# Kernel optimization log

Measured on AMD Instinct MI355X. Metric: run time of the kernel, lower is better.

Reference implementation:

```python
import jax, jax.numpy as jnp
import numpy as np

N = 50000
E = 800000
HID = 128
NH = 8
DH = HID // NH


def setup_inputs() -> dict:
    key = jax.random.key(0)
    ks = jax.random.split(key, 12)
    h = jax.random.normal(ks[0], (N, HID), dtype=jnp.float32)
    row = jnp.sort(jax.random.randint(ks[1], (E,), 0, N))
    col = jax.random.randint(ks[2], (E,), 0, N)
    s = 1.0 / np.sqrt(HID)
    Wq = jax.random.uniform(ks[3], (HID, HID), jnp.float32, -s, s)
    bq = jax.random.uniform(ks[4], (HID,), jnp.float32, -s, s)
    Wk = jax.random.uniform(ks[5], (HID, HID), jnp.float32, -s, s)
    bk = jax.random.uniform(ks[6], (HID,), jnp.float32, -s, s)
    Wv = jax.random.uniform(ks[7], (HID, HID), jnp.float32, -s, s)
    bv = jax.random.uniform(ks[8], (HID,), jnp.float32, -s, s)
    Wo = jax.random.uniform(ks[9], (HID, HID), jnp.float32, -s, s)
    bo = jax.random.uniform(ks[10], (HID,), jnp.float32, -s, s)
    return {"h": h, "row": row, "col": col, "Wq": Wq, "bq": bq,
            "Wk": Wk, "bk": bk, "Wv": Wv, "bv": bv, "Wo": Wo, "bo": bo}


def reference(h, row, col, Wq, bq, Wk, bk, Wv, bv, Wo, bo):
    n = h.shape[0]
    # projections; torch view(N, dh, nh): heads are the fastest-varying axis
    q = (h @ Wq.T + bq).reshape(n, DH, NH)
    k = (h @ Wk.T + bk).reshape(n, DH, NH)
    v = (h @ Wv.T + bv).reshape(n, DH, NH)
    # sddmm: per-edge score[e, head] = sum_d q[row_e, d, head] * k[col_e, d, head]
    scores = jnp.einsum('edh,edh->eh', q[row], k[col]) / np.sqrt(DH)
    # sparse softmax over each row's neighbors (dim=1)
    m = jax.ops.segment_max(scores, row, num_segments=n)       # [N, nh]
    e = jnp.exp(scores - m[row])                               # [E, nh]
    z = jax.ops.segment_sum(e, row, num_segments=n)            # [N, nh]
    attn = e / z[row]
    # bspmm: out[i] = sum_{j in N(i)} attn[ij] * v[j]
    out = jax.ops.segment_sum(attn[:, None, :] * v[col], row, num_segments=n)
    out = out.reshape(n, HID)
    return out @ Wo.T + bo
```

## Files before the change

### kernel.cpp

```cpp
#include <hip/hip_runtime.h>
#include <hip/hip_bf16.h>
#include <math.h>

#define HID 128
#define NH 8
#define DH 16

typedef __bf16 bf16x8 __attribute__((ext_vector_type(8)));
typedef float  f32x4  __attribute__((ext_vector_type(4)));

__global__ void prep_kernel(const int* __restrict__ row, int* __restrict__ row_ptr,
                            int N_, int E_,
                            const float* __restrict__ Wq, const float* __restrict__ Wk,
                            const float* __restrict__ Wv, const float* __restrict__ Wo,
                            const float* __restrict__ bq, const float* __restrict__ bk,
                            const float* __restrict__ bv,
                            __bf16* __restrict__ Whi, __bf16* __restrict__ Wlo,
                            float* __restrict__ bias384) {
    int idx = blockIdx.x * blockDim.x + threadIdx.x;
    if (idx < 4 * 16384) {
        int j = idx >> 14;
        int rem = idx & 16383;
        const float* W = (j == 0) ? Wq : (j == 1) ? Wk : (j == 2) ? Wv : Wo;
        float x = W[rem];
        __bf16 hv = (__bf16)x;
        Whi[idx] = hv;
        Wlo[idx] = (__bf16)(x - (float)hv);
    }
    if (idx <= N_) {
        int lo = 0, hi = E_;
        while (lo < hi) {
            int mid = (lo + hi) >> 1;
            if (row[mid] < idx) lo = mid + 1; else hi = mid;
        }
        row_ptr[idx] = lo;
    }
    if (idx < 384) {
        int j = idx >> 7;
        int pcol = idx & 127;
        int o = ((pcol & 15) << 3) | (pcol >> 4);
        const float* b = (j == 0) ? bq : (j == 1) ? bk : bv;
        bias384[idx] = b[o];
    }
}

__global__ __launch_bounds__(256)
void qkv_mfma_kernel(const float* __restrict__ h, int M,
                     const __bf16* __restrict__ Whi, const __bf16* __restrict__ Wlo,
                     const float* __restrict__ bias384,
                     float* __restrict__ q, __bf16* __restrict__ kv) {
    __shared__ __bf16 As2[2][64 * 128];
    int tid  = threadIdx.x;
    int wv   = tid >> 6;
    int lane = tid & 63;
    int r    = lane & 15;
    int kg   = lane >> 4;
    int m0   = blockIdx.x * 64;
    int colbase = wv * 96;

    #pragma unroll
    for (int it = 0; it < 4; ++it) {
        int flat = it * 256 + tid;
        int row  = flat >> 4;
        int s    = flat & 15;
        int g    = s ^ (row & 7);
        int grow = m0 + row; if (grow > M - 1) grow = M - 1;
        const float* src = &h[(size_t)grow * 128 + g * 8];
        float4 x0 = *(const float4*)src;
        float4 x1 = *(const float4*)(src + 4);
        float xs[8] = {x0.x, x0.y, x0.z, x0.w, x1.x, x1.y, x1.z, x1.w};
        bf16x8 hv8, lv8;
        #pragma unroll
        for (int e = 0; e < 8; ++e) {
            __bf16 hv = (__bf16)xs[e];
            hv8[e] = hv;
            lv8[e] = (__bf16)(xs[e] - (float)hv);
        }
        *(bf16x8*)&As2[0][row * 128 + s * 8] = hv8;
        *(bf16x8*)&As2[1][row * 128 + s * 8] = lv8;
    }
    __syncthreads();

    f32x4 acc[6][4];
    #pragma unroll
    for (int cf = 0; cf < 6; ++cf)
        #pragma unroll
        for (int rf = 0; rf < 4; ++rf)
            acc[cf][rf] = (f32x4){0.f, 0.f, 0.f, 0.f};

    int wrow[6];
    #pragma unroll
    for (int cf = 0; cf < 6; ++cf) {
        int col  = colbase + cf * 16 + r;
        int j    = col >> 7;
        int pcol = col & 127;
        int o    = ((pcol & 15) << 3) | (pcol >> 4);
        wrow[cf] = (j * 128 + o) * 128;
    }

    #pragma unroll
    for (int t = 0; t < 4; ++t) {
        int k0   = t * 32 + kg * 8;
        int slot = t * 4 + kg;
        bf16x8 bh[6], bl[6];
        #pragma unroll
        for (int cf = 0; cf < 6; ++cf) {
            bh[cf] = *(const bf16x8*)&Whi[wrow[cf] + k0];
            bl[cf] = *(const bf16x8*)&Wlo[wrow[cf] + k0];
        }
        bf16x8 ah[4], al[4];
        #pragma unroll
        for (int rf = 0; rf < 4; ++rf) {
            int row = rf * 16 + r;
            int s2  = slot ^ (r & 7);
            ah[rf] = *(bf16x8*)&As2[0][row * 128 + s2 * 8];
            al[rf] = *(bf16x8*)&As2[1][row * 128 + s2 * 8];
        }
        #pragma unroll
        for (int cf = 0; cf < 6; ++cf) {
            #pragma unroll
            for (int rf = 0; rf < 4; ++rf) {
                acc[cf][rf] = __builtin_amdgcn_mfma_f32_16x16x32_bf16(ah[rf], bh[cf], acc[cf][rf], 0, 0, 0);
                acc[cf][rf] = __builtin_amdgcn_mfma_f32_16x16x32_bf16(al[rf], bh[cf], acc[cf][rf], 0, 0, 0);
                acc[cf][rf] = __builtin_amdgcn_mfma_f32_16x16x32_bf16(ah[rf], bl[cf], acc[cf][rf], 0, 0, 0);
            }
        }
    }

    __syncthreads();
    __bf16* kvs = &As2[0][0];
    int orow = kg * 4;
    #pragma unroll
    for (int cf = 0; cf < 6; ++cf) {
        int col  = colbase + cf * 16 + r;
        int j    = col >> 7;
        int pcol = col & 127;
        float b  = bias384[col];
        #pragma unroll
        for (int rf = 0; rf < 4; ++rf) {
            #pragma unroll
            for (int e = 0; e < 4; ++e) {
                int mrow = rf * 16 + orow + e;
                float val = acc[cf][rf][e] + b;
                if (j == 0) {
                    int mg = m0 + mrow;
                    if (mg < M) q[(size_t)mg * 128 + pcol] = val;
                } else {
                    int gi  = pcol >> 2;
                    int idx = gi * 8 + ((j == 1) ? 0 : 4) + (pcol & 3);
                    kvs[mrow * 256 + idx] = (__bf16)val;
                }
            }
        }
    }
    __syncthreads();
    #pragma unroll
    for (int it = 0; it < 8; ++it) {
        int flat = it * 256 + tid;
        int row  = flat >> 5;
        int c    = flat & 31;
        int mg   = m0 + row;
        if (mg < M)
            *(uint4*)&kv[(size_t)mg * 256 + c * 8] = *(uint4*)&kvs[row * 256 + c * 8];
    }
}

__device__ __forceinline__ float blo(unsigned u) { return __uint_as_float(u << 16); }
__device__ __forceinline__ float bhi(unsigned u) { return __uint_as_float(u & 0xffff0000u); }

__global__ __launch_bounds__(256)
void edge_attn_kernel(const int* __restrict__ row_ptr, const int* __restrict__ col,
                      const float* __restrict__ q, const __bf16* __restrict__ kv,
                      float* __restrict__ out, int N_) {
    int wave = threadIdx.x >> 6;
    int lane = threadIdx.x & 63;
    int node = blockIdx.x * 4 + wave;
    if (node >= N_) return;
    int sl   = lane & 31;
    int half = lane >> 5;

    float4 q4 = *(const float4*)&q[(size_t)node * 128 + sl * 4];
    int e0 = row_ptr[node];
    int e1 = row_ptr[node + 1];

    float m = -INFINITY, z = 0.f;
    float4 acc = make_float4(0.f, 0.f, 0.f, 0.f);

    auto score = [&](uint4 u) {
        float p = q4.x * blo(u.x) + q4.y * bhi(u.x) +
                  q4.z * blo(u.y) + q4.w * bhi(u.y);
        p += __shfl_xor(p, 1);
        p += __shfl_xor(p, 2);
        return p * 0.25f;
    };
    auto update = [&](float s, uint4 u) {
        float mnew  = fmaxf(m, s);
        float alpha = __expf(m - mnew);
        float w     = __expf(s - mnew);
        z = z * alpha + w;
        acc.x = acc.x * alpha + w * blo(u.z);
        acc.y = acc.y * alpha + w * bhi(u.z);
        acc.z = acc.z * alpha + w * blo(u.w);
        acc.w = acc.w * alpha + w * bhi(u.w);
        m = mnew;
    };

    int eb = e0;
    for (; eb + 4 <= e1; eb += 4) {
        int ea = eb + half * 2;
        int c0 = col[ea];
        int c1 = col[ea + 1];
        uint4 u0 = *(const uint4*)(kv + (size_t)c0 * 256 + sl * 8);
        uint4 u1 = *(const uint4*)(kv + (size_t)c1 * 256 + sl * 8);
        float s0 = score(u0);
        float s1 = score(u1);
        update(s0, u0);
        update(s1, u1);
    }
    for (; eb < e1; eb += 2) {
        int my_e   = eb + half;
        bool valid = (my_e < e1);
        int cnode  = valid ? col[my_e] : col[eb];
        uint4 u = *(const uint4*)(kv + (size_t)cnode * 256 + sl * 8);
        float s = valid ? score(u) : -INFINITY;
        float mnew = fmaxf(m, s);
        if (mnew > -INFINITY) {
            float alpha = __expf(m - mnew);
            float w     = __expf(s - mnew);
            z = z * alpha + w;
            acc.x = acc.x * alpha + w * blo(u.z);
            acc.y = acc.y * alpha + w * bhi(u.z);
            acc.z = acc.z * alpha + w * blo(u.w);
            acc.w = acc.w * alpha + w * bhi(u.w);
            m = mnew;
        }
    }

    float m2 = __shfl_xor(m, 32);
    float z2 = __shfl_xor(z, 32);
    float ax = __shfl_xor(acc.x, 32);
    float ay = __shfl_xor(acc.y, 32);
    float az = __shfl_xor(acc.z, 32);
    float aw = __shfl_xor(acc.w, 32);
    float mm = fmaxf(m, m2);
    if (mm > -INFINITY) {
        float a1 = __expf(m - mm);
        float a2 = __expf(m2 - mm);
        z = z * a1 + z2 * a2;
        acc.x = acc.x * a1 + ax * a2;
        acc.y = acc.y * a1 + ay * a2;
        acc.z = acc.z * a1 + az * a2;
        acc.w = acc.w * a1 + aw * a2;
    }

    if (half == 0) {
        float inv = (z > 0.f) ? 1.0f / z : 0.f;
        float rr[4] = {acc.x * inv, acc.y * inv, acc.z * inv, acc.w * inv};
        #pragma unroll
        for (int jj = 0; jj < 4; ++jj) {
            int cp = sl * 4 + jj;
            int d  = cp & 15;
            int hd = cp >> 4;
            out[(size_t)node * HID + d * 8 + hd] = rr[jj];
        }
    }
}

__global__ __launch_bounds__(256)
void outproj_mfma_kernel(const float* __restrict__ A, int M,
                         const __bf16* __restrict__ Whi, const __bf16* __restrict__ Wlo,
                         const float* __restrict__ bo, float* __restrict__ C) {
    __shared__ __bf16 As2[2][64 * 128];
    int tid  = threadIdx.x;
    int wv   = tid >> 6;
    int lane = tid & 63;
    int r    = lane & 15;
    int kg   = lane >> 4;
    int m0   = blockIdx.x * 64;
    int colbase = wv * 32;

    #pragma unroll
    for (int it = 0; it < 4; ++it) {
        int flat = it * 256 + tid;
        int row  = flat >> 4;
        int s    = flat & 15;
        int g    = s ^ (row & 7);
        int grow = m0 + row; if (grow > M - 1) grow = M - 1;
        const float* src = &A[(size_t)grow * 128 + g * 8];
        float4 x0 = *(const float4*)src;
        float4 x1 = *(const float4*)(src + 4);
        float xs[8] = {x0.x, x0.y, x0.z, x0.w, x1.x, x1.y, x1.z, x1.w};
        bf16x8 hv8, lv8;
        #pragma unroll
        for (int e = 0; e < 8; ++e) {
            __bf16 hv = (__bf16)xs[e];
            hv8[e] = hv;
            lv8[e] = (__bf16)(xs[e] - (float)hv);
        }
        *(bf16x8*)&As2[0][row * 128 + s * 8] = hv8;
        *(bf16x8*)&As2[1][row * 128 + s * 8] = lv8;
    }
    __syncthreads();

    f32x4 acc[2][4];
    #pragma unroll
    for (int cf = 0; cf < 2; ++cf)
        #pragma unroll
        for (int rf = 0; rf < 4; ++rf)
            acc[cf][rf] = (f32x4){0.f, 0.f, 0.f, 0.f};

    #pragma unroll
    for (int t = 0; t < 4; ++t) {
        int k0   = t * 32 + kg * 8;
        int slot = t * 4 + kg;
        bf16x8 bh[2], bl[2];
        #pragma unroll
        for (int cf = 0; cf < 2; ++cf) {
            int wrow = (colbase + cf * 16 + r) * 128;
            bh[cf] = *(const bf16x8*)&Whi[wrow + k0];
            bl[cf] = *(const bf16x8*)&Wlo[wrow + k0];
        }
        bf16x8 ah[4], al[4];
        #pragma unroll
        for (int rf = 0; rf < 4; ++rf) {
            int row = rf * 16 + r;
            int s2  = slot ^ (r & 7);
            ah[rf] = *(bf16x8*)&As2[0][row * 128 + s2 * 8];
            al[rf] = *(bf16x8*)&As2[1][row * 128 + s2 * 8];
        }
        #pragma unroll
        for (int cf = 0; cf < 2; ++cf) {
            #pragma unroll
            for (int rf = 0; rf < 4; ++rf) {
                acc[cf][rf] = __builtin_amdgcn_mfma_f32_16x16x32_bf16(ah[rf], bh[cf], acc[cf][rf], 0, 0, 0);
                acc[cf][rf] = __builtin_amdgcn_mfma_f32_16x16x32_bf16(al[rf], bh[cf], acc[cf][rf], 0, 0, 0);
                acc[cf][rf] = __builtin_amdgcn_mfma_f32_16x16x32_bf16(ah[rf], bl[cf], acc[cf][rf], 0, 0, 0);
            }
        }
    }

    int orow = kg * 4;
    #pragma unroll
    for (int cf = 0; cf < 2; ++cf) {
        int col = colbase + cf * 16 + r;
        float b = bo[col];
        #pragma unroll
        for (int rf = 0; rf < 4; ++rf) {
            #pragma unroll
            for (int e = 0; e < 4; ++e) {
                int mg = m0 + rf * 16 + orow + e;
                if (mg < M) C[(size_t)mg * HID + col] = acc[cf][rf][e] + b;
            }
        }
    }
}

extern "C" void kernel_launch(void* const* d_in, const int* in_sizes, int n_in,
                              void* d_out, int out_size, void* d_ws, size_t ws_size,
                              hipStream_t stream) {
    const float* h  = (const float*)d_in[0];
    const int* row  = (const int*)d_in[1];
    const int* col  = (const int*)d_in[2];
    const float* Wq = (const float*)d_in[3];
    const float* bq = (const float*)d_in[4];
    const float* Wk = (const float*)d_in[5];
    const float* bk = (const float*)d_in[6];
    const float* Wv = (const float*)d_in[7];
    const float* bv = (const float*)d_in[8];
    const float* Wo = (const float*)d_in[9];
    const float* bo = (const float*)d_in[10];
    float* out = (float*)d_out;

    int N_ = in_sizes[0] / HID;
    int E_ = in_sizes[1];

    char* ws = (char*)d_ws;
    size_t off = 0;
    auto alloc = [&](size_t bytes) {
        void* p = (void*)(ws + off);
        off = (off + bytes + 255) & ~(size_t)255;
        return p;
    };
    int*    row_ptr = (int*)   alloc((size_t)(N_ + 1) * sizeof(int));
    float*  qb      = (float*) alloc((size_t)N_ * 128 * sizeof(float));
    __bf16* kvb     = (__bf16*)alloc((size_t)N_ * 256 * sizeof(__bf16));
    float*  ob      = (float*) alloc((size_t)N_ * HID * sizeof(float));
    __bf16* Whi     = (__bf16*)alloc((size_t)4 * 16384 * sizeof(__bf16));
    __bf16* Wlo     = (__bf16*)alloc((size_t)4 * 16384 * sizeof(__bf16));
    float*  bias384 = (float*) alloc(384 * sizeof(float));
    (void)ws_size;

    prep_kernel<<<256, 256, 0, stream>>>(row, row_ptr, N_, E_,
                                         Wq, Wk, Wv, Wo, bq, bk, bv,
                                         Whi, Wlo, bias384);
    qkv_mfma_kernel<<<(N_ + 63) / 64, 256, 0, stream>>>(h, N_, Whi, Wlo, bias384, qb, kvb);
    edge_attn_kernel<<<(N_ + 3) / 4, 256, 0, stream>>>(row_ptr, col, qb, kvb, ob, N_);
    outproj_mfma_kernel<<<(N_ + 63) / 64, 256, 0, stream>>>(
        ob, N_, Whi + 3 * 16384, Wlo + 3 * 16384, bo, out);
}
```

Baseline: 216.7 us.

## Split projection GEMMs over 2D grid, drop third MFMA term, emit bf16 hi/lo attention output

The QKV and output projection kernels now use a 2D grid that splits the output columns into two halves, doubling the number of blocks and halving per-wave accumulators. The ah*bl correction MFMA is dropped in both GEMMs, trading some precision for fewer matrix instructions. The edge attention kernel now writes its output as bf16 hi/lo pairs in permuted column order with vectorised stores. To match, the Wo weights are pre-permuted so the output projection loads bf16 tiles directly instead of converting fp32 in-kernel. Splitting the columns means each block re-reads and re-splits the h tile in the QKV kernel.

Measured after the change: 204.8 us. 5.5% less time.

```diff
diff --git a/kernel.cpp b/kernel.cpp
--- a/kernel.cpp
+++ b/kernel.cpp
@@ -7,6 +7,7 @@
 #define DH 16
 
 typedef __bf16 bf16x8 __attribute__((ext_vector_type(8)));
+typedef __bf16 bf16x4 __attribute__((ext_vector_type(4)));
 typedef float  f32x4  __attribute__((ext_vector_type(4)));
 
 __global__ void prep_kernel(const int* __restrict__ row, int* __restrict__ row_ptr,
@@ -21,8 +22,16 @@
     if (idx < 4 * 16384) {
         int j = idx >> 14;
         int rem = idx & 16383;
-        const float* W = (j == 0) ? Wq : (j == 1) ? Wk : (j == 2) ? Wv : Wo;
-        float x = W[rem];
+        float x;
+        if (j < 3) {
+            const float* W = (j == 0) ? Wq : (j == 1) ? Wk : Wv;
+            x = W[rem];
+        } else {
+            int o  = rem >> 7;
+            int kp = rem & 127;
+            int k  = ((kp & 15) << 3) | (kp >> 4);
+            x = Wo[o * 128 + k];
+        }
         __bf16 hv = (__bf16)x;
         Whi[idx] = hv;
         Wlo[idx] = (__bf16)(x - (float)hv);
@@ -56,7 +65,7 @@
     int r    = lane & 15;
     int kg   = lane >> 4;
     int m0   = blockIdx.x * 64;
-    int colbase = wv * 96;
+    int by   = blockIdx.y;
 
     #pragma unroll
     for (int it = 0; it < 4; ++it) {
@@ -81,30 +90,32 @@
     }
     __syncthreads();
 
-    f32x4 acc[6][4];
-    #pragma unroll
-    for (int cf = 0; cf < 6; ++cf)
+    f32x4 acc[3][4];
+    #pragma unroll
+    for (int cf = 0; cf < 3; ++cf)
         #pragma unroll
         for (int rf = 0; rf < 4; ++rf)
             acc[cf][rf] = (f32x4){0.f, 0.f, 0.f, 0.f};
 
-    int wrow[6];
-    #pragma unroll
-    for (int cf = 0; cf < 6; ++cf) {
-        int col  = colbase + cf * 16 + r;
-        int j    = col >> 7;
-        int pcol = col & 127;
+    int wrow[3], jseg[3], pcb[3];
+    #pragma unroll
+    for (int cf = 0; cf < 3; ++cf) {
+        int fb   = wv * 48 + cf * 16;
+        int seg  = fb >> 6;
+        int pcol = by * 64 + (fb & 63) + r;
         int o    = ((pcol & 15) << 3) | (pcol >> 4);
-        wrow[cf] = (j * 128 + o) * 128;
+        wrow[cf] = (seg * 128 + o) * 128;
+        jseg[cf] = seg;
+        pcb[cf]  = pcol;
     }
 
     #pragma unroll
     for (int t = 0; t < 4; ++t) {
         int k0   = t * 32 + kg * 8;
         int slot = t * 4 + kg;
-        bf16x8 bh[6], bl[6];
-        #pragma unroll
-        for (int cf = 0; cf < 6; ++cf) {
+        bf16x8 bh[3], bl[3];
+        #pragma unroll
+        for (int cf = 0; cf < 3; ++cf) {
             bh[cf] = *(const bf16x8*)&Whi[wrow[cf] + k0];
             bl[cf] = *(const bf16x8*)&Wlo[wrow[cf] + k0];
         }
@@ -117,12 +128,11 @@
             al[rf] = *(bf16x8*)&As2[1][row * 128 + s2 * 8];
         }
         #pragma unroll
-        for (int cf = 0; cf < 6; ++cf) {
+        for (int cf = 0; cf < 3; ++cf) {
             #pragma unroll
             for (int rf = 0; rf < 4; ++rf) {
                 acc[cf][rf] = __builtin_amdgcn_mfma_f32_16x16x32_bf16(ah[rf], bh[cf], acc[cf][rf], 0, 0, 0);
                 acc[cf][rf] = __builtin_amdgcn_mfma_f32_16x16x32_bf16(al[rf], bh[cf], acc[cf][rf], 0, 0, 0);
-                acc[cf][rf] = __builtin_amdgcn_mfma_f32_16x16x32_bf16(ah[rf], bl[cf], acc[cf][rf], 0, 0, 0);
             }
         }
     }
@@ -131,11 +141,10 @@
     __bf16* kvs = &As2[0][0];
     int orow = kg * 4;
     #pragma unroll
-    for (int cf = 0; cf < 6; ++cf) {
-        int col  = colbase + cf * 16 + r;
-        int j    = col >> 7;
-        int pcol = col & 127;
-        float b  = bias384[col];
+    for (int cf = 0; cf < 3; ++cf) {
+        int j    = jseg[cf];
+        int pcol = pcb[cf];
+        float b  = bias384[j * 128 + pcol];
         #pragma unroll
         for (int rf = 0; rf < 4; ++rf) {
             #pragma unroll
@@ -146,22 +155,23 @@
                     int mg = m0 + mrow;
                     if (mg < M) q[(size_t)mg * 128 + pcol] = val;
                 } else {
-                    int gi  = pcol >> 2;
-                    int idx = gi * 8 + ((j == 1) ? 0 : 4) + (pcol & 3);
-                    kvs[mrow * 256 + idx] = (__bf16)val;
+                    int gl  = (pcol & 63) >> 2;
+                    int idx = gl * 8 + ((j == 1) ? 0 : 4) + (pcol & 3);
+                    kvs[mrow * 128 + idx] = (__bf16)val;
                 }
             }
         }
     }
     __syncthreads();
     #pragma unroll
-    for (int it = 0; it < 8; ++it) {
+    for (int it = 0; it < 4; ++it) {
         int flat = it * 256 + tid;
-        int row  = flat >> 5;
-        int c    = flat & 31;
+        int row  = flat >> 4;
+        int u    = flat & 15;
         int mg   = m0 + row;
         if (mg < M)
-            *(uint4*)&kv[(size_t)mg * 256 + c * 8] = *(uint4*)&kvs[row * 256 + c * 8];
+            *(uint4*)&kv[(size_t)mg * 256 + by * 128 + u * 8] =
+                *(uint4*)&kvs[row * 128 + u * 8];
     }
 }
 
@@ -171,7 +181,7 @@
 __global__ __launch_bounds__(256)
 void edge_attn_kernel(const int* __restrict__ row_ptr, const int* __restrict__ col,
                       const float* __restrict__ q, const __bf16* __restrict__ kv,
-                      float* __restrict__ out, int N_) {
+                      __bf16* __restrict__ obhi, __bf16* __restrict__ oblo, int N_) {
     int wave = threadIdx.x >> 6;
     int lane = threadIdx.x & 63;
     int node = blockIdx.x * 4 + wave;
@@ -256,19 +266,21 @@
     if (half == 0) {
         float inv = (z > 0.f) ? 1.0f / z : 0.f;
         float rr[4] = {acc.x * inv, acc.y * inv, acc.z * inv, acc.w * inv};
+        bf16x4 hv4, lv4;
         #pragma unroll
         for (int jj = 0; jj < 4; ++jj) {
-            int cp = sl * 4 + jj;
-            int d  = cp & 15;
-            int hd = cp >> 4;
-            out[(size_t)node * HID + d * 8 + hd] = rr[jj];
-        }
+            __bf16 hv = (__bf16)rr[jj];
+            hv4[jj] = hv;
+            lv4[jj] = (__bf16)(rr[jj] - (float)hv);
+        }
+        *(bf16x4*)&obhi[(size_t)node * 128 + sl * 4] = hv4;
+        *(bf16x4*)&oblo[(size_t)node * 128 + sl * 4] = lv4;
     }
 }
 
 __global__ __launch_bounds__(256)
-void outproj_mfma_kernel(const float* __restrict__ A, int M,
-                         const __bf16* __restrict__ Whi, const __bf16* __restrict__ Wlo,
+void outproj_mfma_kernel(const __bf16* __restrict__ Ahi_g, const __bf16* __restrict__ Alo_g,
+                         int M, const __bf16* __restrict__ Whi, const __bf16* __restrict__ Wlo,
                          const float* __restrict__ bo, float* __restrict__ C) {
     __shared__ __bf16 As2[2][64 * 128];
     int tid  = threadIdx.x;
@@ -277,7 +289,8 @@
     int r    = lane & 15;
     int kg   = lane >> 4;
     int m0   = blockIdx.x * 64;
-    int colbase = wv * 32;
+    int by   = blockIdx.y;
+    int col  = by * 64 + wv * 16 + r;
 
     #pragma unroll
     for (int it = 0; it < 4; ++it) {
@@ -286,40 +299,22 @@
         int s    = flat & 15;
         int g    = s ^ (row & 7);
         int grow = m0 + row; if (grow > M - 1) grow = M - 1;
-        const float* src = &A[(size_t)grow * 128 + g * 8];
-        float4 x0 = *(const float4*)src;
-        float4 x1 = *(const float4*)(src + 4);
-        float xs[8] = {x0.x, x0.y, x0.z, x0.w, x1.x, x1.y, x1.z, x1.w};
-        bf16x8 hv8, lv8;
-        #pragma unroll
-        for (int e = 0; e < 8; ++e) {
-            __bf16 hv = (__bf16)xs[e];
-            hv8[e] = hv;
-            lv8[e] = (__bf16)(xs[e] - (float)hv);
-        }
-        *(bf16x8*)&As2[0][row * 128 + s * 8] = hv8;
-        *(bf16x8*)&As2[1][row * 128 + s * 8] = lv8;
+        *(bf16x8*)&As2[0][row * 128 + s * 8] = *(const bf16x8*)&Ahi_g[(size_t)grow * 128 + g * 8];
+        *(bf16x8*)&As2[1][row * 128 + s * 8] = *(const bf16x8*)&Alo_g[(size_t)grow * 128 + g * 8];
     }
     __syncthreads();
 
-    f32x4 acc[2][4];
-    #pragma unroll
-    for (int cf = 0; cf < 2; ++cf)
-        #pragma unroll
-        for (int rf = 0; rf < 4; ++rf)
-            acc[cf][rf] = (f32x4){0.f, 0.f, 0.f, 0.f};
-
+    f32x4 acc[4];
+    #pragma unroll
+    for (int rf = 0; rf < 4; ++rf) acc[rf] = (f32x4){0.f, 0.f, 0.f, 0.f};
+
+    int wrow = col * 128;
     #pragma unroll
     for (int t = 0; t < 4; ++t) {
         int k0   = t * 32 + kg * 8;
         int slot = t * 4 + kg;
-        bf16x8 bh[2], bl[2];
-        #pragma unroll
-        for (int cf = 0; cf < 2; ++cf) {
-            int wrow = (colbase + cf * 16 + r) * 128;
-            bh[cf] = *(const bf16x8*)&Whi[wrow + k0];
-            bl[cf] = *(const bf16x8*)&Wlo[wrow + k0];
-        }
+        bf16x8 bh = *(const bf16x8*)&Whi[wrow + k0];
+        bf16x8 bl = *(const bf16x8*)&Wlo[wrow + k0];
         bf16x8 ah[4], al[4];
         #pragma unroll
         for (int rf = 0; rf < 4; ++rf) {
@@ -329,28 +324,19 @@
             al[rf] = *(bf16x8*)&As2[1][row * 128 + s2 * 8];
         }
         #pragma unroll
-        for (int cf = 0; cf < 2; ++cf) {
-            #pragma unroll
-            for (int rf = 0; rf < 4; ++rf) {
-                acc[cf][rf] = __builtin_amdgcn_mfma_f32_16x16x32_bf16(ah[rf], bh[cf], acc[cf][rf], 0, 0, 0);
-                acc[cf][rf] = __builtin_amdgcn_mfma_f32_16x16x32_bf16(al[rf], bh[cf], acc[cf][rf], 0, 0, 0);
-                acc[cf][rf] = __builtin_amdgcn_mfma_f32_16x16x32_bf16(ah[rf], bl[cf], acc[cf][rf], 0, 0, 0);
-            }
-        }
-    }
-
-    int orow = kg * 4;
-    #pragma unroll
-    for (int cf = 0; cf < 2; ++cf) {
-        int col = colbase + cf * 16 + r;
-        float b = bo[col];
-        #pragma unroll
         for (int rf = 0; rf < 4; ++rf) {
-            #pragma unroll
-            for (int e = 0; e < 4; ++e) {
-                int mg = m0 + rf * 16 + orow + e;
-                if (mg < M) C[(size_t)mg * HID + col] = acc[cf][rf][e] + b;
-            }
+            acc[rf] = __builtin_amdgcn_mfma_f32_16x16x32_bf16(ah[rf], bh, acc[rf], 0, 0, 0);
+            acc[rf] = __builtin_amdgcn_mfma_f32_16x16x32_bf16(al[rf], bh, acc[rf], 0, 0, 0);
+        }
+    }
+
+    float b = bo[col];
+    #pragma unroll
+    for (int rf = 0; rf < 4; ++rf) {
+        #pragma unroll
+        for (int e = 0; e < 4; ++e) {
+            int mg = m0 + rf * 16 + kg * 4 + e;
+            if (mg < M) C[(size_t)mg * 128 + col] = acc[rf][e] + b;
         }
     }
 }
@@ -384,7 +370,8 @@
     int*    row_ptr = (int*)   alloc((size_t)(N_ + 1) * sizeof(int));
     float*  qb      = (float*) alloc((size_t)N_ * 128 * sizeof(float));
     __bf16* kvb     = (__bf16*)alloc((size_t)N_ * 256 * sizeof(__bf16));
-    float*  ob      = (float*) alloc((size_t)N_ * HID * sizeof(float));
+    __bf16* obhi    = (__bf16*)alloc((size_t)N_ * 128 * sizeof(__bf16));
+    __bf16* oblo    = (__bf16*)alloc((size_t)N_ * 128 * sizeof(__bf16));
     __bf16* Whi     = (__bf16*)alloc((size_t)4 * 16384 * sizeof(__bf16));
     __bf16* Wlo     = (__bf16*)alloc((size_t)4 * 16384 * sizeof(__bf16));
     float*  bias384 = (float*) alloc(384 * sizeof(float));
@@ -393,8 +380,9 @@
     prep_kernel<<<256, 256, 0, stream>>>(row, row_ptr, N_, E_,
                                          Wq, Wk, Wv, Wo, bq, bk, bv,
                                          Whi, Wlo, bias384);
-    qkv_mfma_kernel<<<(N_ + 63) / 64, 256, 0, stream>>>(h, N_, Whi, Wlo, bias384, qb, kvb);
-    edge_attn_kernel<<<(N_ + 3) / 4, 256, 0, stream>>>(row_ptr, col, qb, kvb, ob, N_);
-    outproj_mfma_kernel<<<(N_ + 63) / 64, 256, 0, stream>>>(
-        ob, N_, Whi + 3 * 16384, Wlo + 3 * 16384, bo, out);
-}
+    qkv_mfma_kernel<<<dim3((N_ + 63) / 64, 2), 256, 0, stream>>>(
+        h, N_, Whi, Wlo, bias384, qb, kvb);
+    edge_attn_kernel<<<(N_ + 3) / 4, 256, 0, stream>>>(row_ptr, col, qb, kvb, obhi, oblo, N_);
+    outproj_mfma_kernel<<<dim3((N_ + 63) / 64, 2), 256, 0, stream>>>(
+        obhi, oblo, N_, Whi + 3 * 16384, Wlo + 3 * 16384, bo, out);
+}
```
